# Optimization experiments

Hardware: AMD Instinct MI355X
Metric: run time of the kernel (lower is better)

The kernel has to match this reference:

```python
import jax, jax.numpy as jnp
import numpy as np

B, N, EPG = 64, 512, 8192
E = B * EPG
K1 = int(np.ceil(0.8 * N))    # 410
K2 = int(np.ceil(0.8 * K1))   # 328


def setup_inputs() -> dict:
    key = jax.random.key(0)
    ks = jax.random.split(key, 32)
    x = jax.random.normal(ks[0], (B * N, 32), jnp.float32)
    edge_attr = jax.random.normal(ks[1], (E, 100), jnp.float32)
    src_l = jax.random.randint(ks[2], (E,), 0, N)
    dst_l = jax.random.randint(ks[3], (E,), 0, N)
    off = jnp.repeat(jnp.arange(B, dtype=jnp.int64) * N, EPG)
    edge_index = jnp.stack([src_l + off, dst_l + off]).astype(jnp.int64)
    batch = jnp.repeat(jnp.arange(B, dtype=jnp.int64), N)

    def lin(k, fin, fout):
        s = 1.0 / np.sqrt(fin)
        k1, k2 = jax.random.split(k)
        return (jax.random.uniform(k1, (fin, fout), jnp.float32, -s, s),
                jax.random.uniform(k2, (fout,), jnp.float32, -s, s))

    dec1_w, dec1_b = lin(ks[4], 100, 64)
    dec2_w, dec2_b = lin(ks[5], 64, 32)
    mlp1_w, mlp1_b = lin(ks[6], 32, 128)
    mlp2_w, mlp2_b = lin(ks[7], 128, 256)
    pool1_w = jax.random.normal(ks[8], (256,), jnp.float32) * 0.1
    gat_w = jax.random.normal(ks[9], (256, 256), jnp.float32) * (1.0 / np.sqrt(256))
    gat_att_src = jax.random.normal(ks[10], (4, 64), jnp.float32) * 0.1
    gat_att_dst = jax.random.normal(ks[11], (4, 64), jnp.float32) * 0.1
    gat_b = jnp.zeros((256,), jnp.float32)
    pool2_w = jax.random.normal(ks[12], (256,), jnp.float32) * 0.1
    lin1_w, lin1_b = lin(ks[13], 512, 128)
    lin2_w, lin2_b = lin(ks[14], 128, 64)
    lin3_w, lin3_b = lin(ks[15], 64, 2)
    return dict(x=x, edge_index=edge_index, batch=batch, edge_attr=edge_attr,
                dec1_w=dec1_w, dec1_b=dec1_b, dec2_w=dec2_w, dec2_b=dec2_b,
                mlp1_w=mlp1_w, mlp1_b=mlp1_b, mlp2_w=mlp2_w, mlp2_b=mlp2_b,
                pool1_w=pool1_w, gat_w=gat_w, gat_att_src=gat_att_src,
                gat_att_dst=gat_att_dst, gat_b=gat_b, pool2_w=pool2_w,
                lin1_w=lin1_w, lin1_b=lin1_b, lin2_w=lin2_w, lin2_b=lin2_b,
                lin3_w=lin3_w, lin3_b=lin3_b)


def _forward(x, edge_attr, dec1_w, dec1_b, dec2_w, dec2_b, mlp1_w, mlp1_b,
             mlp2_w, mlp2_b, pool1_w, gat_w, gat_att_src, gat_att_dst, gat_b,
             pool2_w, lin1_w, lin1_b, lin2_w, lin2_b, lin3_w, lin3_b,
             src, dst):
    # edge encoder
    ea = jax.nn.relu(edge_attr @ dec1_w + dec1_b)
    ea = jax.nn.relu(ea @ dec2_w + dec2_b)                       # [E,32]
    # GINEConv (eps=0): sum_j relu(x_j + e_ji), then mlp((1+eps)x + aggr)
    msg = jax.nn.relu(x[src] + ea)
    agg = jax.ops.segment_sum(msg, dst, num_segments=B * N)
    h = x + agg
    h = jax.nn.relu(h @ mlp1_w + mlp1_b) @ mlp2_w + mlp2_b       # [BN,256]
    h = jax.nn.relu(h)
    # TopKPooling 1 (uniform graphs -> fixed k)
    s = jnp.tanh((h @ pool1_w) / jnp.linalg.norm(pool1_w))       # [BN]
    topv, topi = jax.lax.top_k(s.reshape(B, N), K1)              # [B,K1]
    gperm = (topi + jnp.arange(B)[:, None] * N).reshape(-1)
    hp = h[gperm] * topv.reshape(-1)[:, None]                    # [B*K1,256]
    kept = jnp.zeros(B * N, bool).at[gperm].set(True)
    newid = jnp.zeros(B * N, jnp.int32).at[gperm].set(jnp.arange(B * K1, dtype=jnp.int32))
    src1, dst1 = newid[src], newid[dst]
    valid = kept[src] & kept[dst]
    # readout 1: global max + mean pool
    hr = hp.reshape(B, K1, 256)
    x1 = jnp.concatenate([hr.max(axis=1), hr.mean(axis=1)], axis=-1)  # [B,512]
    # GATConv(256, 64, heads=4) with self-loops; invalid edges masked
    Nk = B * K1
    loops = jnp.arange(Nk, dtype=jnp.int32)
    src2 = jnp.concatenate([src1, loops])
    dst2 = jnp.concatenate([dst1, loops])
    valid2 = jnp.concatenate([valid, jnp.ones(Nk, bool)])
    xl = (hp @ gat_w).reshape(Nk, 4, 64)
    a_src = (xl * gat_att_src).sum(-1)                           # [Nk,4]
    a_dst = (xl * gat_att_dst).sum(-1)
    logit = jax.nn.leaky_relu(a_src[src2] + a_dst[dst2], 0.2)    # [E2,4]
    logit = jnp.where(valid2[:, None], logit, -jnp.inf)
    m = jax.ops.segment_max(logit, dst2, num_segments=Nk)
    e = jnp.where(valid2[:, None], jnp.exp(logit - m[dst2]), 0.0)
    den = jax.ops.segment_sum(e, dst2, num_segments=Nk)
    alpha = e / den[dst2]
    out = jax.ops.segment_sum(alpha[:, :, None] * xl[src2], dst2, num_segments=Nk)
    g = jax.nn.relu(out.reshape(Nk, 256) + gat_b)
    # TopKPooling 2 (pooled edges unused downstream)
    s2 = jnp.tanh((g @ pool2_w) / jnp.linalg.norm(pool2_w))
    topv2, topi2 = jax.lax.top_k(s2.reshape(B, K1), K2)
    gperm2 = (topi2 + jnp.arange(B)[:, None] * K1).reshape(-1)
    gp = (g[gperm2] * topv2.reshape(-1)[:, None]).reshape(B, K2, 256)
    x2 = jnp.concatenate([gp.max(axis=1), gp.mean(axis=1)], axis=-1)
    # head (dropout = identity in eval)
    z = x1 + x2
    z = jax.nn.relu(z @ lin1_w + lin1_b)
    z = jax.nn.relu(z @ lin2_w + lin2_b)
    return jax.nn.log_softmax(z @ lin3_w + lin3_b, axis=-1)     # [B,2]


def reference(x, edge_index, batch, edge_attr, dec1_w, dec1_b, dec2_w, dec2_b,
              mlp1_w, mlp1_b, mlp2_w, mlp2_b, pool1_w, gat_w, gat_att_src,
              gat_att_dst, gat_b, pool2_w, lin1_w, lin1_b, lin2_w, lin2_b,
              lin3_w, lin3_b):
    src = edge_index[0].astype(jnp.int32)
    dst = edge_index[1].astype(jnp.int32)
    return _forward(x, edge_attr, dec1_w, dec1_b, dec2_w, dec2_b, mlp1_w,
                    mlp1_b, mlp2_w, mlp2_b, pool1_w, gat_w, gat_att_src,
                    gat_att_dst, gat_b, pool2_w, lin1_w, lin1_b, lin2_w,
                    lin2_b, lin3_w, lin3_b, src, dst)
```

## Files before the change

kernel.cpp:

```cpp
#include <hip/hip_runtime.h>
#include <math.h>

#define B_   64
#define N_   512
#define E_   524288
#define BN_  32768
#define K1_  410
#define K2_  328
#define NK_  26240
#define KC_  25

__device__ __forceinline__ float lrelu(float x) { return x > 0.f ? x : 0.2f * x; }

__global__ __launch_bounds__(256) void norm_kernel(const float* __restrict__ p1,
                                                   const float* __restrict__ p2,
                                                   float* __restrict__ norms) {
    __shared__ float r1[256], r2[256];
    int t = threadIdx.x;
    float a = p1[t], b = p2[t];
    r1[t] = a * a; r2[t] = b * b;
    for (int o = 128; o > 0; o >>= 1) {
        __syncthreads();
        if (t < o) { r1[t] += r1[t + o]; r2[t] += r2[t + o]; }
    }
    __syncthreads();
    if (t == 0) { norms[0] = sqrtf(r1[0]); norms[1] = sqrtf(r2[0]); }
}

template <int NSEG>
__global__ __launch_bounds__(1024) void scan_kernel(int* __restrict__ cnt, int* __restrict__ offsets)
{
    __shared__ int part[1024];
    int t = threadIdx.x;
    const int CH = (NSEG + 1023) / 1024;
    int base = t * CH;
    int sum = 0;
    for (int i = 0; i < CH; ++i) { int gi = base + i; if (gi < NSEG) sum += cnt[gi]; }
    part[t] = sum;
    __syncthreads();
    for (int o = 1; o < 1024; o <<= 1) {
        int v = (t >= o) ? part[t - o] : 0;
        __syncthreads();
        part[t] += v;
        __syncthreads();
    }
    int run = (t == 0) ? 0 : part[t - 1];
    for (int i = 0; i < CH; ++i) {
        int gi = base + i;
        if (gi < NSEG) { offsets[gi] = run; run += cnt[gi]; cnt[gi] = 0; }
    }
    if (t == 1023) offsets[NSEG] = part[1023];
}

__global__ __launch_bounds__(256) void count_node_kernel(const int* __restrict__ dstG,
                                                         int* __restrict__ cnt_node)
{
    int e = blockIdx.x * blockDim.x + threadIdx.x;
    atomicAdd(&cnt_node[dstG[e]], 1);
}

__global__ __launch_bounds__(256) void fill_node_kernel(const int* __restrict__ dstG,
                                                        const int* __restrict__ offs_node,
                                                        int* __restrict__ cnt_node,
                                                        int* __restrict__ csr_e)
{
    int e = blockIdx.x * blockDim.x + threadIdx.x;
    int d = dstG[e];
    int p = offs_node[d] + atomicAdd(&cnt_node[d], 1);
    csr_e[p] = e;
}

__global__ __launch_bounds__(256) void edge_mlp_agg_kernel(
    const float* __restrict__ edge_attr, const int* __restrict__ srcG,
    const int* __restrict__ dstG, const int* __restrict__ csr_e,
    const float* __restrict__ x,
    const float* __restrict__ W1, const float* __restrict__ b1,
    const float* __restrict__ W2, const float* __restrict__ b2,
    float* __restrict__ agg)
{
    __shared__ float bufAT[KC_][68];
    __shared__ float w1cT[KC_][64];
    __shared__ float ea1T[64][68];
    __shared__ float w2s[64][32];
    __shared__ float b2s[32];
    __shared__ int   srcs[64], dsts[64], eid_s[64];

    int tid = threadIdx.x;
    int eb  = blockIdx.x * 64;

    if (tid < 64) {
        int e = csr_e[eb + tid];
        eid_s[tid] = e;
        srcs[tid]  = srcG[e];
        dsts[tid]  = dstG[e];
    }
    for (int i = tid; i < 64 * 32; i += 256) w2s[i >> 5][i & 31] = W2[i];
    if (tid >= 192 && tid < 224) b2s[tid - 192] = b2[tid - 192];

    int tx = tid & 15, ty = tid >> 4;
    float b1v[4];
#pragma unroll
    for (int j = 0; j < 4; ++j) b1v[j] = b1[tx * 4 + j];

    float acc[4][4] = {};
    __syncthreads();

    float raA[7], raB[7], rw[7];
    auto issueA = [&](int kc, float (&ra)[7]) {
#pragma unroll
        for (int u = 0; u < 7; ++u) {
            int i = tid + u * 256;
            if (i < 1600) {
                int e = i / 25, k = i - e * 25;
                ra[u] = edge_attr[(size_t)eid_s[e] * 100 + kc + k];
            }
        }
    };
    auto issueW = [&](int kc) {
#pragma unroll
        for (int u = 0; u < 7; ++u) {
            int i = tid + u * 256;
            if (i < 1600) rw[u] = W1[(size_t)(kc + (i >> 6)) * 64 + (i & 63)];
        }
    };
    auto lwriteA = [&](float (&ra)[7]) {
#pragma unroll
        for (int u = 0; u < 7; ++u) {
            int i = tid + u * 256;
            if (i < 1600) {
                int e = i / 25, k = i - e * 25;
                bufAT[k][e] = ra[u];
            }
        }
    };
    auto lwriteW = [&]() {
#pragma unroll
        for (int u = 0; u < 7; ++u) {
            int i = tid + u * 256;
            if (i < 1600) w1cT[i >> 6][i & 63] = rw[u];
        }
    };

    issueA(0, raA);
    issueW(0);
    issueA(KC_, raB);
    lwriteA(raA); lwriteW();
    __syncthreads();

#pragma unroll
    for (int c = 0; c < 4; ++c) {
        if (c == 0) issueA(2 * KC_, raA);
        if (c == 1) issueA(3 * KC_, raB);
        if (c < 3)  issueW((c + 1) * KC_);
#pragma unroll 5
        for (int k = 0; k < KC_; ++k) {
            float4 a4 = *(const float4*)&bufAT[k][ty * 4];
            float4 w4 = *(const float4*)&w1cT[k][tx * 4];
            float a[4] = { a4.x, a4.y, a4.z, a4.w };
            float w[4] = { w4.x, w4.y, w4.z, w4.w };
#pragma unroll
            for (int i = 0; i < 4; ++i)
#pragma unroll
                for (int j = 0; j < 4; ++j) acc[i][j] += a[i] * w[j];
        }
        if (c < 3) {
            __syncthreads();
            if ((c & 1) == 0) lwriteA(raB);
            else              lwriteA(raA);
            lwriteW();
            __syncthreads();
        }
    }
#pragma unroll
    for (int j = 0; j < 4; ++j) {
        float4 v;
        v.x = fmaxf(acc[0][j] + b1v[j], 0.f);
        v.y = fmaxf(acc[1][j] + b1v[j], 0.f);
        v.z = fmaxf(acc[2][j] + b1v[j], 0.f);
        v.w = fmaxf(acc[3][j] + b1v[j], 0.f);
        *(float4*)&ea1T[tx * 4 + j][ty * 4] = v;
    }
    __syncthreads();

    int e0 = (tid >> 3) * 2;
    int c0 = (tid & 7) * 4;
    float acc2[2][4] = {};
    for (int k = 0; k < 64; ++k) {
        float2 a2 = *(const float2*)&ea1T[k][e0];
        float4 w4 = *(const float4*)&w2s[k][c0];
        float w[4] = { w4.x, w4.y, w4.z, w4.w };
#pragma unroll
        for (int j = 0; j < 4; ++j) {
            acc2[0][j] += a2.x * w[j]; acc2[1][j] += a2.y * w[j];
        }
    }
    __syncthreads();
#pragma unroll
    for (int r = 0; r < 2; ++r) {
        int e = e0 + r, s = srcs[e];
        const float4 xv = *(const float4*)(x + (size_t)s * 32 + c0);
        float xa[4] = { xv.x, xv.y, xv.z, xv.w };
        float4 m;
        m.x = fmaxf(xa[0] + fmaxf(acc2[r][0] + b2s[c0 + 0], 0.f), 0.f);
        m.y = fmaxf(xa[1] + fmaxf(acc2[r][1] + b2s[c0 + 1], 0.f), 0.f);
        m.z = fmaxf(xa[2] + fmaxf(acc2[r][2] + b2s[c0 + 2], 0.f), 0.f);
        m.w = fmaxf(xa[3] + fmaxf(acc2[r][3] + b2s[c0 + 3], 0.f), 0.f);
        *(float4*)&ea1T[e][c0] = m;
    }
    __syncthreads();

    int grp = tid >> 3, gc = (tid & 7) * 4;
    for (int e = grp; e < 64; e += 32) {
        if (e > 0 && dsts[e] == dsts[e - 1]) continue;
        int d = dsts[e];
        float s0 = 0.f, s1 = 0.f, s2 = 0.f, s3 = 0.f;
        for (int j = e; j < 64 && dsts[j] == d; ++j) {
            float2 p0 = *(const float2*)&ea1T[j][gc];
            float2 p1 = *(const float2*)&ea1T[j][gc + 2];
            s0 += p0.x; s1 += p0.y; s2 += p1.x; s3 += p1.y;
        }
        atomicAdd(&agg[(size_t)d * 32 + gc + 0], s0);
        atomicAdd(&agg[(size_t)d * 32 + gc + 1], s1);
        atomicAdd(&agg[(size_t)d * 32 + gc + 2], s2);
        atomicAdd(&agg[(size_t)d * 32 + gc + 3], s3);
    }
}

template <int ACT, bool HASBIAS, bool HASA2>
__global__ __launch_bounds__(256) void gemm_tile128(
    const float* __restrict__ A, const float* __restrict__ A2,
    const float* __restrict__ W, const float* __restrict__ bias,
    float* __restrict__ C, int M, int N, int K)
{
    __shared__ float As[16][132];
    __shared__ float Ws[16][132];
    int tid = threadIdx.x;
    int tx = tid & 15, ty = tid >> 4;
    int mb = blockIdx.y * 128, nb = blockIdx.x * 128;
    float acc[8][8] = {};

    int am = tid & 127;
    int ak = (tid >> 7) * 8;
    int wk = tid >> 4;
    int wn = (tid & 15) * 8;

    for (int kt = 0; kt < K; kt += 16) {
        {
            const float* pa = A + (size_t)(mb + am) * K + kt + ak;
            float4 v0 = *(const float4*)(pa);
            float4 v1 = *(const float4*)(pa + 4);
            if (HASA2) {
                const float* pb = A2 + (size_t)(mb + am) * K + kt + ak;
                float4 u0 = *(const float4*)(pb);
                float4 u1 = *(const float4*)(pb + 4);
                v0.x += u0.x; v0.y += u0.y; v0.z += u0.z; v0.w += u0.w;
                v1.x += u1.x; v1.y += u1.y; v1.z += u1.z; v1.w += u1.w;
            }
            As[ak + 0][am] = v0.x; As[ak + 1][am] = v0.y;
            As[ak + 2][am] = v0.z; As[ak + 3][am] = v0.w;
            As[ak + 4][am] = v1.x; As[ak + 5][am] = v1.y;
            As[ak + 6][am] = v1.z; As[ak + 7][am] = v1.w;
        }
        {
            const float* pw = W + (size_t)(kt + wk) * N + nb + wn;
            *(float4*)&Ws[wk][wn]     = *(const float4*)(pw);
            *(float4*)&Ws[wk][wn + 4] = *(const float4*)(pw + 4);
        }
        __syncthreads();
#pragma unroll
        for (int k2 = 0; k2 < 16; ++k2) {
            float4 a0 = *(const float4*)&As[k2][ty * 8];
            float4 a1 = *(const float4*)&As[k2][ty * 8 + 4];
            float4 w0 = *(const float4*)&Ws[k2][tx * 4];
            float4 w1 = *(const float4*)&Ws[k2][64 + tx * 4];
            float a[8] = { a0.x, a0.y, a0.z, a0.w, a1.x, a1.y, a1.z, a1.w };
            float w[8] = { w0.x, w0.y, w0.z, w0.w, w1.x, w1.y, w1.z, w1.w };
#pragma unroll
            for (int i = 0; i < 8; ++i)
#pragma unroll
                for (int j = 0; j < 8; ++j) acc[i][j] += a[i] * w[j];
        }
        __syncthreads();
    }
#pragma unroll
    for (int i = 0; i < 8; ++i) {
        int m = mb + ty * 8 + i;
        int col0 = nb + tx * 4, col1 = nb + 64 + tx * 4;
        float r[8];
#pragma unroll
        for (int j = 0; j < 4; ++j) {
            float v = acc[i][j];
            if (HASBIAS) v += bias[col0 + j];
            if (ACT == 1) v = fmaxf(v, 0.f);
            r[j] = v;
        }
#pragma unroll
        for (int j = 4; j < 8; ++j) {
            float v = acc[i][j];
            if (HASBIAS) v += bias[col1 + j - 4];
            if (ACT == 1) v = fmaxf(v, 0.f);
            r[j] = v;
        }
        float4 o0 = { r[0], r[1], r[2], r[3] };
        float4 o1 = { r[4], r[5], r[6], r[7] };
        *(float4*)&C[(size_t)m * N + col0] = o0;
        *(float4*)&C[(size_t)m * N + col1] = o1;
    }
}

__global__ __launch_bounds__(256) void scores_kernel(const float* __restrict__ P,
                                                     const float* __restrict__ w,
                                                     const float* __restrict__ norms, int nidx,
                                                     float* __restrict__ s, int R)
{
    int wid  = (blockIdx.x * blockDim.x + threadIdx.x) >> 6;
    int lane = threadIdx.x & 63;
    if (wid >= R) return;
    float acc = 0.f;
#pragma unroll
    for (int r = 0; r < 4; ++r) {
        int d = r * 64 + lane;
        acc += P[(size_t)wid * 256 + d] * w[d];
    }
    for (int o = 32; o > 0; o >>= 1) acc += __shfl_xor(acc, o);
    if (lane == 0) s[wid] = tanhf(acc / norms[nidx]);
}

__device__ void bitonic_desc512(float* val, int* idx, int t) {
    for (int k = 2; k <= 512; k <<= 1) {
        for (int j = k >> 1; j > 0; j >>= 1) {
            __syncthreads();
            int ixj = t ^ j;
            if (ixj > t) {
                float v0 = val[t], v1 = val[ixj];
                int   i0 = idx[t], i1 = idx[ixj];
                bool before = (v0 > v1) || (v0 == v1 && i0 < i1);
                bool dir = ((t & k) == 0);
                bool doswap = dir ? (!before) : before;
                if (doswap) { val[t] = v1; val[ixj] = v0; idx[t] = i1; idx[ixj] = i0; }
            }
        }
    }
    __syncthreads();
}

__global__ __launch_bounds__(512) void topk1_kernel(const float* __restrict__ s,
                                                    float* __restrict__ topval,
                                                    int* __restrict__ topnode,
                                                    int* __restrict__ kept,
                                                    int* __restrict__ newid)
{
    __shared__ float val[512];
    __shared__ int   idx[512];
    int b = blockIdx.x, t = threadIdx.x;
    val[t] = s[b * N_ + t]; idx[t] = t;
    bitonic_desc512(val, idx, t);
    if (t < K1_) {
        int node = b * N_ + idx[t];
        int orow = b * K1_ + t;
        topnode[orow] = node;
        topval[orow]  = val[t];
        kept[node]  = 1;
        newid[node] = orow;
    }
}

__global__ __launch_bounds__(256) void gather_scale_kernel(const float* __restrict__ h,
                                                           const int* __restrict__ topnode,
                                                           const float* __restrict__ topval,
                                                           float* __restrict__ hp)
{
    int gid = blockIdx.x * blockDim.x + threadIdx.x;
    int row = gid >> 6, q = gid & 63;
    float4 v = *(const float4*)(h + (size_t)topnode[row] * 256 + q * 4);
    float tv = topval[row];
    float4 o; o.x = v.x * tv; o.y = v.y * tv; o.z = v.z * tv; o.w = v.w * tv;
    *(float4*)(hp + (size_t)row * 256 + q * 4) = o;
}

__global__ __launch_bounds__(1024) void readout1_kernel(const float* __restrict__ hp,
                                                        float* __restrict__ zbuf)
{
    __shared__ float rmx[1024], rsm[1024];
    int b = blockIdx.x >> 2, cg = blockIdx.x & 3;
    int tid = threadIdx.x;
    int cl = tid & 63, rg = tid >> 6;
    int c = cg * 64 + cl;
    float mx = -INFINITY, sm = 0.f;
    for (int j = rg; j < K1_; j += 16) {
        float v = hp[((size_t)b * K1_ + j) * 256 + c];
        mx = fmaxf(mx, v); sm += v;
    }
    rmx[tid] = mx; rsm[tid] = sm;
    __syncthreads();
    if (tid < 512) { rmx[tid] = fmaxf(rmx[tid], rmx[tid + 512]); rsm[tid] += rsm[tid + 512]; }
    __syncthreads();
    if (tid < 256) { rmx[tid] = fmaxf(rmx[tid], rmx[tid + 256]); rsm[tid] += rsm[tid + 256]; }
    __syncthreads();
    if (tid < 128) { rmx[tid] = fmaxf(rmx[tid], rmx[tid + 128]); rsm[tid] += rsm[tid + 128]; }
    __syncthreads();
    if (tid < 64) {
        zbuf[b * 512 + c]       = fmaxf(rmx[tid], rmx[tid + 64]);
        zbuf[b * 512 + 256 + c] = (rsm[tid] + rsm[tid + 64]) / (float)K1_;
    }
}

__global__ __launch_bounds__(256) void attcoef_kernel(const float* __restrict__ xl,
                                                      const float* __restrict__ att_src,
                                                      const float* __restrict__ att_dst,
                                                      float* __restrict__ a_src,
                                                      float* __restrict__ a_dst)
{
    int wid  = (blockIdx.x * blockDim.x + threadIdx.x) >> 6;
    int lane = threadIdx.x & 63;
    if (wid >= NK_) return;
    float vs[4], vd[4];
#pragma unroll
    for (int r = 0; r < 4; ++r) {
        int d = r * 64 + lane;
        float v = xl[(size_t)wid * 256 + d];
        vs[r] = v * att_src[d];
        vd[r] = v * att_dst[d];
    }
    for (int o = 32; o > 0; o >>= 1) {
#pragma unroll
        for (int r = 0; r < 4; ++r) {
            vs[r] += __shfl_xor(vs[r], o);
            vd[r] += __shfl_xor(vd[r], o);
        }
    }
    if (lane == 0) {
#pragma unroll
        for (int r = 0; r < 4; ++r) {
            a_src[wid * 4 + r] = vs[r];
            a_dst[wid * 4 + r] = vd[r];
        }
    }
}

__global__ __launch_bounds__(256) void count_kernel(const int* __restrict__ srcG,
                                                    const int* __restrict__ dstG,
                                                    const int* __restrict__ kept,
                                                    const int* __restrict__ newid,
                                                    int* __restrict__ cnt)
{
    int e = blockIdx.x * blockDim.x + threadIdx.x;
    int s = srcG[e], d = dstG[e];
    if (kept[s] && kept[d]) atomicAdd(&cnt[newid[d]], 1);
}

__global__ __launch_bounds__(256) void fill_kernel(const int* __restrict__ srcG,
                                                   const int* __restrict__ dstG,
                                                   const int* __restrict__ kept,
                                                   const int* __restrict__ newid,
                                                   const int* __restrict__ offsets,
                                                   int* __restrict__ cnt,
                                                   int* __restrict__ csr_src)
{
    int e = blockIdx.x * blockDim.x + threadIdx.x;
    int s = srcG[e], d = dstG[e];
    if (kept[s] && kept[d]) {
        int d1 = newid[d];
        int p = offsets[d1] + atomicAdd(&cnt[d1], 1);
        csr_src[p] = newid[s];
    }
}

__global__ __launch_bounds__(256) void gat_agg_kernel(const float* __restrict__ xl,
                                                      const float* __restrict__ a_src,
                                                      const float* __restrict__ a_dst,
                                                      const int* __restrict__ offsets,
                                                      const int* __restrict__ csr_src,
                                                      const float* __restrict__ gat_b,
                                                      const float* __restrict__ pool2_w,
                                                      const float* __restrict__ norms,
                                                      float* __restrict__ g,
                                                      float* __restrict__ s2)
{
    int wid  = (blockIdx.x * blockDim.x + threadIdx.x) >> 6;
    int lane = threadIdx.x & 63;
    if (wid >= NK_) return;
    int off0 = offsets[wid], off1 = offsets[wid + 1];

    float4 ad = *(const float4*)(a_dst + (size_t)wid * 4);
    float4 asf = *(const float4*)(a_src + (size_t)wid * 4);
    float adv[4] = { ad.x, ad.y, ad.z, ad.w };
    float lsf[4] = { lrelu(asf.x + ad.x), lrelu(asf.y + ad.y),
                     lrelu(asf.z + ad.z), lrelu(asf.w + ad.w) };

    float mx[4] = { lsf[0], lsf[1], lsf[2], lsf[3] };
    for (int e = off0 + lane; e < off1; e += 64) {
        int s1 = csr_src[e];
        float4 a = *(const float4*)(a_src + (size_t)s1 * 4);
        float av[4] = { a.x, a.y, a.z, a.w };
#pragma unroll
        for (int r = 0; r < 4; ++r) mx[r] = fmaxf(mx[r], lrelu(av[r] + adv[r]));
    }
    for (int o = 32; o > 0; o >>= 1)
#pragma unroll
        for (int r = 0; r < 4; ++r) mx[r] = fmaxf(mx[r], __shfl_xor(mx[r], o));

    float den[4] = {};
    float acc[4] = {};
    int s_next = (off0 < off1) ? csr_src[off0] : 0;
    for (int e = off0; e < off1; ++e) {
        int s1 = s_next;
        if (e + 1 < off1) s_next = csr_src[e + 1];
        float4 a = *(const float4*)(a_src + (size_t)s1 * 4);
        float av[4] = { a.x, a.y, a.z, a.w };
#pragma unroll
        for (int r = 0; r < 4; ++r) {
            float w = expf(lrelu(av[r] + adv[r]) - mx[r]);
            den[r] += w;
            acc[r] += w * xl[(size_t)s1 * 256 + r * 64 + lane];
        }
    }
    float gv[4];
#pragma unroll
    for (int r = 0; r < 4; ++r) {
        float ws = expf(lsf[r] - mx[r]);
        den[r] += ws;
        acc[r] = (acc[r] + ws * xl[(size_t)wid * 256 + r * 64 + lane]) / den[r];
        int d = r * 64 + lane;
        gv[r] = fmaxf(acc[r] + gat_b[d], 0.f);
        g[(size_t)wid * 256 + d] = gv[r];
    }
    float dot = 0.f;
#pragma unroll
    for (int r = 0; r < 4; ++r) dot += gv[r] * pool2_w[r * 64 + lane];
    for (int o = 32; o > 0; o >>= 1) dot += __shfl_xor(dot, o);
    if (lane == 0) s2[wid] = tanhf(dot / norms[1]);
}

__global__ __launch_bounds__(512) void topk2_sort_kernel(const float* __restrict__ s2,
                                                         int* __restrict__ t2row,
                                                         float* __restrict__ t2val)
{
    __shared__ float val[512];
    __shared__ int   idx[512];
    int b = blockIdx.x, t = threadIdx.x;
    val[t] = (t < K1_) ? s2[b * K1_ + t] : -INFINITY;
    idx[t] = t;
    bitonic_desc512(val, idx, t);
    if (t < K2_) {
        t2row[b * K2_ + t] = b * K1_ + idx[t];
        t2val[b * K2_ + t] = val[t];
    }
}

__global__ __launch_bounds__(512) void readout2_kernel(const float* __restrict__ g,
                                                       const int* __restrict__ t2row,
                                                       const float* __restrict__ t2val,
                                                       float* __restrict__ zbuf)
{
    __shared__ float rmx[512], rsm[512];
    int b = blockIdx.x >> 2, cg = blockIdx.x & 3;
    int tid = threadIdx.x;
    int cl = tid & 63, rg = tid >> 6;
    int c = cg * 64 + cl;
    float mx = -INFINITY, sm = 0.f;
    for (int j = rg; j < K2_; j += 8) {
        int row = t2row[b * K2_ + j];
        float v = g[(size_t)row * 256 + c] * t2val[b * K2_ + j];
        mx = fmaxf(mx, v); sm += v;
    }
    rmx[tid] = mx; rsm[tid] = sm;
    __syncthreads();
    if (tid < 256) { rmx[tid] = fmaxf(rmx[tid], rmx[tid + 256]); rsm[tid] += rsm[tid + 256]; }
    __syncthreads();
    if (tid < 128) { rmx[tid] = fmaxf(rmx[tid], rmx[tid + 128]); rsm[tid] += rsm[tid + 128]; }
    __syncthreads();
    if (tid < 64) {
        zbuf[b * 512 + c]       += fmaxf(rmx[tid], rmx[tid + 64]);
        zbuf[b * 512 + 256 + c] += (rsm[tid] + rsm[tid + 64]) / (float)K2_;
    }
}

__global__ __launch_bounds__(128) void head_kernel(const float* __restrict__ zbuf,
                                                   const float* __restrict__ l1w, const float* __restrict__ l1b,
                                                   const float* __restrict__ l2w, const float* __restrict__ l2b,
                                                   const float* __restrict__ l3w, const float* __restrict__ l3b,
                                                   float* __restrict__ out)
{
    __shared__ float zs[512];
    __shared__ float h1s[128];
    __shared__ float h2s[64];
    __shared__ float os[2];
    int b = blockIdx.x, t = threadIdx.x;
    for (int i = t; i < 512; i += 128) zs[i] = zbuf[b * 512 + i];
    __syncthreads();
    float acc = l1b[t];
    for (int k = 0; k < 512; ++k) acc += zs[k] * l1w[k * 128 + t];
    h1s[t] = fmaxf(acc, 0.f);
    __syncthreads();
    if (t < 64) {
        float a2 = l2b[t];
        for (int k = 0; k < 128; ++k) a2 += h1s[k] * l2w[k * 64 + t];
        h2s[t] = fmaxf(a2, 0.f);
    }
    __syncthreads();
    if (t < 2) {
        float a3 = l3b[t];
        for (int k = 0; k < 64; ++k) a3 += h2s[k] * l3w[k * 2 + t];
        os[t] = a3;
    }
    __syncthreads();
    if (t == 0) {
        float m = fmaxf(os[0], os[1]);
        float lse = m + logf(expf(os[0] - m) + expf(os[1] - m));
        out[b * 2 + 0] = os[0] - lse;
        out[b * 2 + 1] = os[1] - lse;
    }
}

extern "C" void kernel_launch(void* const* d_in, const int* in_sizes, int n_in,
                              void* d_out, int out_size, void* d_ws, size_t ws_size,
                              hipStream_t stream)
{
    const float* x         = (const float*)d_in[0];
    const int*   eidx      = (const int*)d_in[1];
    const float* edge_attr = (const float*)d_in[3];
    const float* dec1_w    = (const float*)d_in[4];
    const float* dec1_b    = (const float*)d_in[5];
    const float* dec2_w    = (const float*)d_in[6];
    const float* dec2_b    = (const float*)d_in[7];
    const float* mlp1_w    = (const float*)d_in[8];
    const float* mlp1_b    = (const float*)d_in[9];
    const float* mlp2_w    = (const float*)d_in[10];
    const float* mlp2_b    = (const float*)d_in[11];
    const float* pool1_w   = (const float*)d_in[12];
    const float* gat_w     = (const float*)d_in[13];
    const float* att_src   = (const float*)d_in[14];
    const float* att_dst   = (const float*)d_in[15];
    const float* gat_b     = (const float*)d_in[16];
    const float* pool2_w   = (const float*)d_in[17];
    const float* lin1_w    = (const float*)d_in[18];
    const float* lin1_b    = (const float*)d_in[19];
    const float* lin2_w    = (const float*)d_in[20];
    const float* lin2_b    = (const float*)d_in[21];
    const float* lin3_w    = (const float*)d_in[22];
    const float* lin3_b    = (const float*)d_in[23];
    const int* srcG = eidx;
    const int* dstG = eidx + E_;
    float* out = (float*)d_out;

    char* base = (char*)d_ws;
    size_t o = 0;
    auto alloc = [&](size_t bytes) { size_t r = o; o = (o + bytes + 255) & ~(size_t)255; return r; };
    size_t agg_off    = alloc((size_t)BN_ * 32 * 4);
    size_t cntn_off   = alloc((size_t)BN_ * 4);
    size_t cnt_off    = alloc((size_t)NK_ * 4);
    size_t kept_off   = alloc((size_t)BN_ * 4);
    size_t zero_bytes = o;
    size_t newid_off  = alloc((size_t)BN_ * 4);
    size_t offsn_off  = alloc((size_t)(BN_ + 1) * 4);
    size_t csre_off   = alloc((size_t)E_ * 4);
    size_t h_off      = alloc((size_t)BN_ * 256 * 4);
    size_t hp_off     = alloc((size_t)NK_ * 256 * 4);
    size_t xl_off     = alloc((size_t)NK_ * 256 * 4);
    size_t s_off      = alloc((size_t)BN_ * 4);
    size_t tnode_off  = alloc((size_t)NK_ * 4);
    size_t tval_off   = alloc((size_t)NK_ * 4);
    size_t offs_off   = alloc((size_t)(NK_ + 1) * 4);
    size_t csr_off    = alloc((size_t)E_ * 4);
    size_t zbuf_off   = alloc((size_t)B_ * 512 * 4);
    size_t asrc_off   = alloc((size_t)NK_ * 4 * 4);
    size_t adst_off   = alloc((size_t)NK_ * 4 * 4);
    size_t norm_off   = alloc(256);
    if (o > ws_size) return;

    float* agg      = (float*)(base + agg_off);
    int*   cnt_node = (int*)  (base + cntn_off);
    int*   cnt      = (int*)  (base + cnt_off);
    int*   kept     = (int*)  (base + kept_off);
    int*   newid    = (int*)  (base + newid_off);
    int*   offs_n   = (int*)  (base + offsn_off);
    int*   csr_e    = (int*)  (base + csre_off);
    float* h        = (float*)(base + h_off);
    float* g        = h;
    float* hp       = (float*)(base + hp_off);
    float* xl       = (float*)(base + xl_off);
    float* t1       = xl;
    float* s        = (float*)(base + s_off);
    int*   tnode    = (int*)  (base + tnode_off);
    float* tval     = (float*)(base + tval_off);
    int*   offs     = (int*)  (base + offs_off);
    int*   csr      = (int*)  (base + csr_off);
    float* zbuf     = (float*)(base + zbuf_off);
    float* a_src    = (float*)(base + asrc_off);
    float* a_dst    = (float*)(base + adst_off);
    float* norms    = (float*)(base + norm_off);

    hipMemsetAsync(d_ws, 0, zero_bytes, stream);

    norm_kernel<<<1, 256, 0, stream>>>(pool1_w, pool2_w, norms);

    count_node_kernel<<<E_ / 256, 256, 0, stream>>>(dstG, cnt_node);
    scan_kernel<BN_><<<1, 1024, 0, stream>>>(cnt_node, offs_n);
    fill_node_kernel<<<E_ / 256, 256, 0, stream>>>(dstG, offs_n, cnt_node, csr_e);

    edge_mlp_agg_kernel<<<E_ / 64, 256, 0, stream>>>(edge_attr, srcG, dstG, csr_e, x,
                                                     dec1_w, dec1_b, dec2_w, dec2_b, agg);

    gemm_tile128<1, true, true><<<dim3(128 / 128, BN_ / 128), 256, 0, stream>>>(
        x, agg, mlp1_w, mlp1_b, t1, BN_, 128, 32);
    gemm_tile128<1, true, false><<<dim3(256 / 128, BN_ / 128), 256, 0, stream>>>(
        t1, nullptr, mlp2_w, mlp2_b, h, BN_, 256, 128);

    scores_kernel<<<BN_ / 4, 256, 0, stream>>>(h, pool1_w, norms, 0, s, BN_);
    topk1_kernel<<<B_, 512, 0, stream>>>(s, tval, tnode, kept, newid);
    gather_scale_kernel<<<(NK_ * 64) / 256, 256, 0, stream>>>(h, tnode, tval, hp);
    readout1_kernel<<<B_ * 4, 1024, 0, stream>>>(hp, zbuf);

    gemm_tile128<0, false, false><<<dim3(256 / 128, NK_ / 128), 256, 0, stream>>>(
        hp, nullptr, gat_w, nullptr, xl, NK_, 256, 256);
    attcoef_kernel<<<NK_ / 4, 256, 0, stream>>>(xl, att_src, att_dst, a_src, a_dst);

    count_kernel<<<E_ / 256, 256, 0, stream>>>(srcG, dstG, kept, newid, cnt);
    scan_kernel<NK_><<<1, 1024, 0, stream>>>(cnt, offs);
    fill_kernel<<<E_ / 256, 256, 0, stream>>>(srcG, dstG, kept, newid, offs, cnt, csr);

    gat_agg_kernel<<<NK_ / 4, 256, 0, stream>>>(xl, a_src, a_dst, offs, csr, gat_b,
                                                pool2_w, norms, g, s);

    topk2_sort_kernel<<<B_, 512, 0, stream>>>(s, tnode, tval);
    readout2_kernel<<<B_ * 4, 512, 0, stream>>>(g, tnode, tval, zbuf);

    head_kernel<<<B_, 128, 0, stream>>>(zbuf, lin1_w, lin1_b, lin2_w, lin2_b,
                                        lin3_w, lin3_b, out);
}
```

Baseline: 598.4 us.

## Process edges in natural order, scatter messages sorted, then segment-sum per node

The edge MLP kernel now reads edge_attr contiguously in original edge order instead of gathering rows through a dst-sorted permutation, and writes each message to its sorted position in a buffer that aliases h. A new segment-sum kernel then reduces each node's contiguous message range without atomics, replacing the in-block run detection and global float atomicAdds. The GAT aggregation loop is also unrolled by two to overlap independent gathers. The cost is an extra 64 MB write and read of the message buffer plus one more launch, and the removed barriers depend on the srcs/poss shared arrays being published by later syncs.

```diff
diff --git a/kernel.cpp b/kernel.cpp
--- a/kernel.cpp
+++ b/kernel.cpp
@@ -62,38 +62,33 @@
 __global__ __launch_bounds__(256) void fill_node_kernel(const int* __restrict__ dstG,
                                                         const int* __restrict__ offs_node,
                                                         int* __restrict__ cnt_node,
-                                                        int* __restrict__ csr_e)
+                                                        int* __restrict__ pos_e)
 {
     int e = blockIdx.x * blockDim.x + threadIdx.x;
     int d = dstG[e];
     int p = offs_node[d] + atomicAdd(&cnt_node[d], 1);
-    csr_e[p] = e;
-}
-
-__global__ __launch_bounds__(256) void edge_mlp_agg_kernel(
+    pos_e[e] = p;
+}
+
+__global__ __launch_bounds__(256) void edge_mlp_kernel(
     const float* __restrict__ edge_attr, const int* __restrict__ srcG,
-    const int* __restrict__ dstG, const int* __restrict__ csr_e,
+    const int* __restrict__ pos_e,
     const float* __restrict__ x,
     const float* __restrict__ W1, const float* __restrict__ b1,
     const float* __restrict__ W2, const float* __restrict__ b2,
-    float* __restrict__ agg)
+    float* __restrict__ msg_sorted)
 {
     __shared__ float bufAT[KC_][68];
     __shared__ float w1cT[KC_][64];
     __shared__ float ea1T[64][68];
     __shared__ float w2s[64][32];
     __shared__ float b2s[32];
-    __shared__ int   srcs[64], dsts[64], eid_s[64];
+    __shared__ int   srcs[64], poss[64];
 
     int tid = threadIdx.x;
     int eb  = blockIdx.x * 64;
 
-    if (tid < 64) {
-        int e = csr_e[eb + tid];
-        eid_s[tid] = e;
-        srcs[tid]  = srcG[e];
-        dsts[tid]  = dstG[e];
-    }
+    if (tid < 64) { srcs[tid] = srcG[eb + tid]; poss[tid] = pos_e[eb + tid]; }
     for (int i = tid; i < 64 * 32; i += 256) w2s[i >> 5][i & 31] = W2[i];
     if (tid >= 192 && tid < 224) b2s[tid - 192] = b2[tid - 192];
 
@@ -103,7 +98,6 @@
     for (int j = 0; j < 4; ++j) b1v[j] = b1[tx * 4 + j];
 
     float acc[4][4] = {};
-    __syncthreads();
 
     float raA[7], raB[7], rw[7];
     auto issueA = [&](int kc, float (&ra)[7]) {
@@ -112,7 +106,7 @@
             int i = tid + u * 256;
             if (i < 1600) {
                 int e = i / 25, k = i - e * 25;
-                ra[u] = edge_attr[(size_t)eid_s[e] * 100 + kc + k];
+                ra[u] = edge_attr[(size_t)(eb + e) * 100 + kc + k];
             }
         }
     };
@@ -194,7 +188,6 @@
             acc2[0][j] += a2.x * w[j]; acc2[1][j] += a2.y * w[j];
         }
     }
-    __syncthreads();
 #pragma unroll
     for (int r = 0; r < 2; ++r) {
         int e = e0 + r, s = srcs[e];
@@ -205,25 +198,24 @@
         m.y = fmaxf(xa[1] + fmaxf(acc2[r][1] + b2s[c0 + 1], 0.f), 0.f);
         m.z = fmaxf(xa[2] + fmaxf(acc2[r][2] + b2s[c0 + 2], 0.f), 0.f);
         m.w = fmaxf(xa[3] + fmaxf(acc2[r][3] + b2s[c0 + 3], 0.f), 0.f);
-        *(float4*)&ea1T[e][c0] = m;
-    }
-    __syncthreads();
-
-    int grp = tid >> 3, gc = (tid & 7) * 4;
-    for (int e = grp; e < 64; e += 32) {
-        if (e > 0 && dsts[e] == dsts[e - 1]) continue;
-        int d = dsts[e];
-        float s0 = 0.f, s1 = 0.f, s2 = 0.f, s3 = 0.f;
-        for (int j = e; j < 64 && dsts[j] == d; ++j) {
-            float2 p0 = *(const float2*)&ea1T[j][gc];
-            float2 p1 = *(const float2*)&ea1T[j][gc + 2];
-            s0 += p0.x; s1 += p0.y; s2 += p1.x; s3 += p1.y;
-        }
-        atomicAdd(&agg[(size_t)d * 32 + gc + 0], s0);
-        atomicAdd(&agg[(size_t)d * 32 + gc + 1], s1);
-        atomicAdd(&agg[(size_t)d * 32 + gc + 2], s2);
-        atomicAdd(&agg[(size_t)d * 32 + gc + 3], s3);
-    }
+        *(float4*)(msg_sorted + (size_t)poss[e] * 32 + c0) = m;
+    }
+}
+
+__global__ __launch_bounds__(256) void segsum_kernel(const float* __restrict__ msg_sorted,
+                                                     const int* __restrict__ offs_n,
+                                                     float* __restrict__ agg)
+{
+    int wid  = (blockIdx.x * blockDim.x + threadIdx.x) >> 6;
+    int lane = threadIdx.x & 63;
+    if (wid >= BN_) return;
+    int off0 = offs_n[wid], off1 = offs_n[wid + 1];
+    int col = lane & 31, rr = lane >> 5;
+    float sum = 0.f;
+    for (int j = off0 + rr; j < off1; j += 2)
+        sum += msg_sorted[(size_t)j * 32 + col];
+    sum += __shfl_xor(sum, 32);
+    if (lane < 32) agg[(size_t)wid * 32 + col] = sum;
 }
 
 template <int ACT, bool HASBIAS, bool HASA2>
@@ -502,17 +494,32 @@
 
     float den[4] = {};
     float acc[4] = {};
-    int s_next = (off0 < off1) ? csr_src[off0] : 0;
-    for (int e = off0; e < off1; ++e) {
-        int s1 = s_next;
-        if (e + 1 < off1) s_next = csr_src[e + 1];
-        float4 a = *(const float4*)(a_src + (size_t)s1 * 4);
-        float av[4] = { a.x, a.y, a.z, a.w };
+    int e = off0;
+    for (; e + 1 < off1; e += 2) {
+        int s1 = csr_src[e], s2v = csr_src[e + 1];
+        float4 a1 = *(const float4*)(a_src + (size_t)s1 * 4);
+        float4 a2 = *(const float4*)(a_src + (size_t)s2v * 4);
+        float av1[4] = { a1.x, a1.y, a1.z, a1.w };
+        float av2[4] = { a2.x, a2.y, a2.z, a2.w };
 #pragma unroll
         for (int r = 0; r < 4; ++r) {
-            float w = expf(lrelu(av[r] + adv[r]) - mx[r]);
-            den[r] += w;
-            acc[r] += w * xl[(size_t)s1 * 256 + r * 64 + lane];
+            float w1 = expf(lrelu(av1[r] + adv[r]) - mx[r]);
+            float w2 = expf(lrelu(av2[r] + adv[r]) - mx[r]);
+            float x1 = xl[(size_t)s1 * 256 + r * 64 + lane];
+            float x2 = xl[(size_t)s2v * 256 + r * 64 + lane];
+            den[r] += w1 + w2;
+            acc[r] += w1 * x1 + w2 * x2;
+        }
+    }
+    if (e < off1) {
+        int s1 = csr_src[e];
+        float4 a1 = *(const float4*)(a_src + (size_t)s1 * 4);
+        float av1[4] = { a1.x, a1.y, a1.z, a1.w };
+#pragma unroll
+        for (int r = 0; r < 4; ++r) {
+            float w1 = expf(lrelu(av1[r] + adv[r]) - mx[r]);
+            den[r] += w1;
+            acc[r] += w1 * xl[(size_t)s1 * 256 + r * 64 + lane];
         }
     }
     float gv[4];
@@ -654,7 +661,7 @@
     size_t zero_bytes = o;
     size_t newid_off  = alloc((size_t)BN_ * 4);
     size_t offsn_off  = alloc((size_t)(BN_ + 1) * 4);
-    size_t csre_off   = alloc((size_t)E_ * 4);
+    size_t pos_off    = alloc((size_t)E_ * 4);
     size_t h_off      = alloc((size_t)BN_ * 256 * 4);
     size_t hp_off     = alloc((size_t)NK_ * 256 * 4);
     size_t xl_off     = alloc((size_t)NK_ * 256 * 4);
@@ -675,9 +682,10 @@
     int*   kept     = (int*)  (base + kept_off);
     int*   newid    = (int*)  (base + newid_off);
     int*   offs_n   = (int*)  (base + offsn_off);
-    int*   csr_e    = (int*)  (base + csre_off);
+    int*   pos_e    = (int*)  (base + pos_off);
     float* h        = (float*)(base + h_off);
     float* g        = h;
+    float* msg      = h;
     float* hp       = (float*)(base + hp_off);
     float* xl       = (float*)(base + xl_off);
     float* t1       = xl;
@@ -697,10 +705,11 @@
 
     count_node_kernel<<<E_ / 256, 256, 0, stream>>>(dstG, cnt_node);
     scan_kernel<BN_><<<1, 1024, 0, stream>>>(cnt_node, offs_n);
-    fill_node_kernel<<<E_ / 256, 256, 0, stream>>>(dstG, offs_n, cnt_node, csr_e);
-
-    edge_mlp_agg_kernel<<<E_ / 64, 256, 0, stream>>>(edge_attr, srcG, dstG, csr_e, x,
-                                                     dec1_w, dec1_b, dec2_w, dec2_b, agg);
+    fill_node_kernel<<<E_ / 256, 256, 0, stream>>>(dstG, offs_n, cnt_node, pos_e);
+
+    edge_mlp_kernel<<<E_ / 64, 256, 0, stream>>>(edge_attr, srcG, pos_e, x,
+                                                 dec1_w, dec1_b, dec2_w, dec2_b, msg);
+    segsum_kernel<<<BN_ / 4, 256, 0, stream>>>(msg, offs_n, agg);
 
     gemm_tile128<1, true, true><<<dim3(128 / 128, BN_ / 128), 256, 0, stream>>>(
         x, agg, mlp1_w, mlp1_b, t1, BN_, 128, 32);
```

New measurement: 578.2 us. -3.4%, faster.
